# Optimization experiments

Measured on AMD Instinct MI355X. Metric: run time of the kernel, lower is better.

Reference implementation:

```python
import jax, jax.numpy as jnp
import numpy as np

T_CONST = 0.1

def _hardtanh(w):
    # F.hardtanh(w, min_val=1e-10, max_val=1)
    return jnp.clip(w, 1e-10, 1.0)

def _forward(inp, hn, w_str2str, w_str2snr, w_m12m1, w_m12str, w_thal2m1,
             w_m12thal, w_thal2str, w_str2stn, w_stn2snr, w_snr2thal,
             str2str_fixed, inp_weight, mean_w, mean_b, std_w, std_b, hid_dim):
    H = hid_dim
    H5 = 5 * H
    Z = jnp.zeros((H, H), dtype=inp.dtype)
    n_inhib = int(0.3 * H)

    # Diagonal 'D' matrices realized as column scalings (D is diagonal)
    m12m1_d = jnp.concatenate([jnp.ones((H - n_inhib,)), -jnp.ones((n_inhib,))])

    # Block masks
    str2str_mask = jnp.zeros((H, H))
    m12str_mask = jnp.concatenate([jnp.ones((H, H - n_inhib)), jnp.zeros((H, n_inhib))], axis=1)
    str2stn_mask = jnp.concatenate([jnp.zeros((H, H // 2)), jnp.ones((H, H // 2))], axis=1)
    str2snr_mask = jnp.concatenate([jnp.ones((H, H // 2)), jnp.zeros((H, H // 2))], axis=1)

    # Region masks over the full 5H state
    thal_mask = jnp.concatenate([jnp.zeros((3 * H,)), jnp.ones((H,)), jnp.zeros((H,))])
    m1_mask = jnp.zeros((H5,))  # cat(zeros(4H), zeros(H)) in the source

    # Effective recurrent blocks (str2str_D = stn2snr_D = snr2thal_D = str2snr_D = -I)
    str2str_rec = -(str2str_mask * _hardtanh(w_str2str) + str2str_fixed)
    m12m1_rec = _hardtanh(w_m12m1) * m12m1_d[None, :]
    m12str_rec = m12str_mask * _hardtanh(w_m12str)
    str2snr_rec = -(str2snr_mask * _hardtanh(w_str2snr))
    thal2m1_rec = _hardtanh(w_thal2m1)
    m12thal_rec = _hardtanh(w_m12thal)
    thal2str_rec = _hardtanh(w_thal2str)
    str2stn_rec = str2stn_mask * _hardtanh(w_str2stn)
    stn2snr_rec = -_hardtanh(w_str2stn)  # NOTE: source uses str2stn weight here (faithful to original)
    snr2thal_rec = -_hardtanh(w_snr2thal)

    W_rec = jnp.concatenate([
        jnp.concatenate([str2str_rec, Z, Z, thal2str_rec, m12str_rec], axis=1),
        jnp.concatenate([str2stn_rec, Z, Z, Z, Z], axis=1),
        jnp.concatenate([str2snr_rec, stn2snr_rec, Z, Z, Z], axis=1),
        jnp.concatenate([Z, Z, snr2thal_rec, Z, m12thal_rec], axis=1),
        jnp.concatenate([Z, Z, Z, thal2m1_rec, m12m1_rec], axis=1),
    ], axis=0)  # [5H, 5H]

    # Precompute masked input drive for all timesteps: [T, B, 5H]
    u = jnp.einsum('bti,ih->tbh', inp, _hardtanh(inp_weight)) * thal_mask

    W_rec_T = W_rec.T

    def step(h, u_t):
        # (W_rec @ h.T).T == h @ W_rec.T
        h_new = jax.nn.relu((1.0 - T_CONST) * h + T_CONST * (h @ W_rec_T + u_t))
        return h_new, h_new

    _, hs = jax.lax.scan(step, hn[0], u)  # hs: [T, B, 5H]
    rnn_out = jnp.transpose(hs, (1, 0, 2))  # [B, T, 5H]
    hn_last = rnn_out[:, -1, :][None]  # [1, B, 5H]

    masked = rnn_out * m1_mask
    mean_out = masked @ mean_w + mean_b
    std_out = jnp.clip(masked @ std_w + std_b, -5.0, 10.0)
    return mean_out, std_out, rnn_out, hn_last


def setup_inputs() -> dict:
    H, B, T, I, A = 256, 64, 512, 4, 1
    H5 = 5 * H
    key = jax.random.key(0)
    ks = jax.random.split(key, 20)
    u01 = lambda k, shape, s: jax.random.uniform(k, shape, dtype=jnp.float32) * s
    inputs = {
        'inp': jax.random.uniform(ks[0], (B, T, I), dtype=jnp.float32),
        'hn': jnp.zeros((1, B, H5), dtype=jnp.float32),
        'w_str2str': u01(ks[1], (H, H), 0.01),
        'w_str2snr': u01(ks[2], (H, H), 0.01),
        'w_m12m1': u01(ks[3], (H, H), 0.01),
        'w_m12str': u01(ks[4], (H, H), 0.01),
        'w_thal2m1': u01(ks[5], (H, H), 0.01),
        'w_m12thal': u01(ks[6], (H, H), 0.01),
        'w_thal2str': u01(ks[7], (H, H), 0.01),
        'w_str2stn': u01(ks[8], (H, H), 0.01),
        'w_stn2snr': u01(ks[9], (H, H), 0.01),
        'w_snr2thal': u01(ks[10], (H, H), 0.01),
        'inp_weight': u01(ks[12], (I, H5), 0.1),
        'mean_w': jax.random.normal(ks[13], (H5, A), dtype=jnp.float32) * 0.02,
        'mean_b': jnp.zeros((A,), dtype=jnp.float32),
        'std_w': jax.random.normal(ks[14], (H5, A), dtype=jnp.float32) * 0.02,
        'std_b': jnp.zeros((A,), dtype=jnp.float32),
        'hid_dim': H,
    }
    keep = jax.random.bernoulli(ks[11], 0.15, (H, H)).astype(jnp.float32)
    inputs['str2str_fixed'] = u01(ks[15], (H, H), 0.01) * keep
    return inputs


def reference(inp, hn, w_str2str, w_str2snr, w_m12m1, w_m12str, w_thal2m1,
              w_m12thal, w_thal2str, w_str2stn, w_stn2snr, w_snr2thal,
              str2str_fixed, inp_weight, mean_w, mean_b, std_w, std_b, hid_dim):
    return _forward(inp, hn, w_str2str, w_str2snr, w_m12m1, w_m12str, w_thal2m1,
                    w_m12thal, w_thal2str, w_str2stn, w_stn2snr, w_snr2thal,
                    str2str_fixed, inp_weight, mean_w, mean_b, std_w, std_b, hid_dim)
```

## Files before the change

### kernel.cpp

```cpp
#include <hip/hip_runtime.h>

typedef unsigned short u16;
typedef unsigned long long u64;
typedef __bf16 v8bf __attribute__((ext_vector_type(8)));
typedef float f32x4 __attribute__((ext_vector_type(4)));
typedef u16 u16x4 __attribute__((ext_vector_type(4)));

#define H5 1280
#define TT 512
#define NBLK 80
#define GBLK 20
#define SPL 81920

#define OFF_W0 0
#define OFF_W1 3276800
#define OFF_W2 6553600
#define OFF_HS 9830400
#define OFF_WIN 10813440
#define OFF_CNT 10817536

#define MFMA(a, b, c) __builtin_amdgcn_mfma_f32_16x16x32_bf16(a, b, c, 0, 0, 0)

__device__ __forceinline__ float htanh_(float x) {
  return fminf(fmaxf(x, 1e-10f), 1.0f);
}
__device__ __forceinline__ u16 f2b(float f) {
  unsigned u = __float_as_uint(f);
  return (u16)((u + 0x7fffu + ((u >> 16) & 1u)) >> 16);
}
__device__ __forceinline__ float b2f(u16 b) {
  return __uint_as_float(((unsigned)b) << 16);
}

__device__ __forceinline__ v8bf ldh16(const u16* p) {
  v8bf v;
  asm volatile("global_load_dwordx4 %0, %1, off sc0 sc1" : "=v"(v) : "v"(p) : "memory");
  return v;
}
__device__ __forceinline__ void sth(u16* p, u16x4 v) {
  union { u16x4 s; u64 q; } u;
  u.s = v;
  __hip_atomic_store((u64*)p, u.q, __ATOMIC_RELAXED, __HIP_MEMORY_SCOPE_AGENT);
}

__global__ void build_w(const float* __restrict__ w_str2snr, const float* __restrict__ w_m12m1,
                        const float* __restrict__ w_m12str, const float* __restrict__ w_thal2m1,
                        const float* __restrict__ w_m12thal, const float* __restrict__ w_thal2str,
                        const float* __restrict__ w_str2stn, const float* __restrict__ w_snr2thal,
                        const float* __restrict__ fixedw, u16* __restrict__ W0,
                        u16* __restrict__ W1, u16* __restrict__ W2) {
  int idx = blockIdx.x * 256 + threadIdx.x;
  if (idx >= H5 * H5) return;
  int j = idx / H5, k = idx - j * H5;
  int jr = j >> 8, kr = k >> 8, kk = k & 255;
  int o = (j & 255) * 256 + kk;
  float w = 0.0f;
  if (jr == 0) {
    if (kr == 0) w = -fixedw[o];
    else if (kr == 3) w = htanh_(w_thal2str[o]);
    else if (kr == 4) w = (kk < 180) ? htanh_(w_m12str[o]) : 0.0f;
  } else if (jr == 1) {
    if (kr == 0) w = (kk >= 128) ? htanh_(w_str2stn[o]) : 0.0f;
  } else if (jr == 2) {
    if (kr == 0) w = (kk < 128) ? -htanh_(w_str2snr[o]) : 0.0f;
    else if (kr == 1) w = -htanh_(w_str2stn[o]);
  } else if (jr == 3) {
    if (kr == 2) w = -htanh_(w_snr2thal[o]);
    else if (kr == 4) w = htanh_(w_m12thal[o]);
  } else {
    if (kr == 3) w = htanh_(w_thal2m1[o]);
    else if (kr == 4) w = (kk < 180) ? htanh_(w_m12m1[o]) : -htanh_(w_m12m1[o]);
  }
  u16 c0 = f2b(w);  float r1 = w - b2f(c0);
  u16 c1 = f2b(r1); float r2 = r1 - b2f(c1);
  u16 c2 = f2b(r2);
  W0[idx] = c0; W1[idx] = c1; W2[idx] = c2;
}

__global__ void build_misc(const float* __restrict__ hn, const float* __restrict__ inp_weight,
                           const float* __restrict__ mean_b, const float* __restrict__ std_b,
                           float* __restrict__ out, u16* __restrict__ hs, float* __restrict__ Win) {
  int gid = blockIdx.x * 256 + threadIdx.x;
  if (gid < 65536) {
    out[gid] = (gid < 32768) ? mean_b[0] : fminf(10.0f, fmaxf(-5.0f, std_b[0]));
  } else if (gid < 65536 + SPL) {
    int i = gid - 65536;
    float v = hn[i];
    u16 c0 = f2b(v);  float r1 = v - b2f(c0);
    u16 c1 = f2b(r1); float r2 = r1 - b2f(c1);
    u16 c2 = f2b(r2);
    hs[i] = c0; hs[SPL + i] = c1; hs[2 * SPL + i] = c2;
  } else if (gid < 65536 + SPL + 1024) {
    int i = gid - 65536 - SPL;
    Win[i] = htanh_(inp_weight[(i >> 8) * H5 + 768 + (i & 255)]);
  }
}

template <int R> struct RC;
template <> struct RC<0> { static constexpr int kb[3] = {0, 768, 1024}; static constexpr int nch[3] = {8, 8, 8}; };
template <> struct RC<1> { static constexpr int kb[3] = {128, 0, 0};    static constexpr int nch[3] = {4, 0, 0}; };
template <> struct RC<2> { static constexpr int kb[3] = {0, 256, 0};    static constexpr int nch[3] = {4, 8, 0}; };
template <> struct RC<3> { static constexpr int kb[3] = {512, 1024, 0}; static constexpr int nch[3] = {8, 8, 0}; };
template <> struct RC<4> { static constexpr int kb[3] = {768, 1024, 0}; static constexpr int nch[3] = {8, 8, 0}; };

template <int R>
__device__ __forceinline__ f32x4 do_mm(const u16* __restrict__ hs_r, int b, int lk,
                                       const u16* __restrict__ w0r, const u16* __restrict__ w1r,
                                       const u16* __restrict__ w2r) {
  f32x4 A00 = {0.f, 0.f, 0.f, 0.f}, A01 = {0.f, 0.f, 0.f, 0.f}, A02 = {0.f, 0.f, 0.f, 0.f};
  f32x4 A10 = {0.f, 0.f, 0.f, 0.f}, A11 = {0.f, 0.f, 0.f, 0.f}, A20 = {0.f, 0.f, 0.f, 0.f};
#pragma unroll
  for (int q = 0; q < 3; ++q) {
    if (RC<R>::nch[q] > 0) {
      const int kbq = RC<R>::kb[q];
      const u16* hb = hs_r + (long)b * H5 + kbq + lk;
      v8bf h0[8], h1[8], h2[8];
#pragma unroll
      for (int c = 0; c < RC<R>::nch[q]; ++c) {
        h0[c] = ldh16(hb + c * 32);
        h1[c] = ldh16(hb + SPL + c * 32);
        h2[c] = ldh16(hb + 2 * SPL + c * 32);
      }
      asm volatile("s_waitcnt vmcnt(0)" ::: "memory");
      __builtin_amdgcn_sched_barrier(0);
#pragma unroll
      for (int c = 0; c < RC<R>::nch[q]; ++c) {
        v8bf a0 = *(const v8bf*)(w0r + kbq + c * 32);
        v8bf a1 = *(const v8bf*)(w1r + kbq + c * 32);
        v8bf a2 = *(const v8bf*)(w2r + kbq + c * 32);
        A00 = MFMA(a0, h0[c], A00);
        A01 = MFMA(a0, h1[c], A01);
        A02 = MFMA(a0, h2[c], A02);
        A10 = MFMA(a1, h0[c], A10);
        A11 = MFMA(a1, h1[c], A11);
        A20 = MFMA(a2, h0[c], A20);
      }
    }
  }
  f32x4 acc;
#pragma unroll
  for (int rr = 0; rr < 4; ++rr)
    acc[rr] = ((A00[rr] + A10[rr]) + (A01[rr] + A11[rr])) + (A02[rr] + A20[rr]);
  return acc;
}

template <int R>
__device__ void pers_loop(int j0, int b, int lr, int hi, int lk,
                          const float* __restrict__ inp_b, const float* __restrict__ hn,
                          const u16* __restrict__ W0, const u16* __restrict__ W1,
                          const u16* __restrict__ W2, u16* __restrict__ hs,
                          float* __restrict__ rnn_b, float* __restrict__ hn_last,
                          const float* __restrict__ Win, unsigned* __restrict__ ctr) {
  const long jrow = (long)(j0 + lr) * H5 + lk;
  const u16* w0r = W0 + jrow;
  const u16* w1r = W1 + jrow;
  const u16* w2r = W2 + jrow;

  float winreg[4][4];
  if constexpr (R == 3) {
#pragma unroll
    for (int i = 0; i < 4; ++i)
#pragma unroll
      for (int rr = 0; rr < 4; ++rr)
        winreg[i][rr] = Win[i * 256 + (j0 - 768) + hi * 4 + rr];
  }

  f32x4 hprev;
  {
    const float* hp = hn + (long)b * H5 + j0 + hi * 4;
#pragma unroll
    for (int rr = 0; rr < 4; ++rr) hprev[rr] = hp[rr];
  }

  const u64 ca = (u64)ctr;

  for (int t = 0; t < TT; ++t) {
    const u16* hs_r = hs + (t & 1) * (3 * SPL);
    u16* hs_w = hs + ((t & 1) ^ 1) * (3 * SPL);

    f32x4 acc = do_mm<R>(hs_r, b, lk, w0r, w1r, w2r);

    if constexpr (R == 3) {
      const float* ip = inp_b + t * 4;
      float i0 = ip[0], i1 = ip[1], i2 = ip[2], i3 = ip[3];
#pragma unroll
      for (int rr = 0; rr < 4; ++rr)
        acc[rr] += i0 * winreg[0][rr] + i1 * winreg[1][rr] + i2 * winreg[2][rr] + i3 * winreg[3][rr];
    }

    f32x4 hnew;
#pragma unroll
    for (int rr = 0; rr < 4; ++rr)
      hnew[rr] = fmaxf(0.0f, 0.9f * hprev[rr] + 0.1f * acc[rr]);
    hprev = hnew;

    *(f32x4*)(rnn_b + (long)t * H5 + j0 + hi * 4) = hnew;

    if (t < TT - 1) {
      u16x4 s0, s1, s2;
#pragma unroll
      for (int rr = 0; rr < 4; ++rr) {
        float v = hnew[rr];
        u16 c0 = f2b(v);  float r1 = v - b2f(c0);
        u16 c1 = f2b(r1); float r2 = r1 - b2f(c1);
        s0[rr] = c0; s1[rr] = c1; s2[rr] = f2b(r2);
      }
      u16* hw = hs_w + (long)b * H5 + j0 + hi * 4;
      sth(hw, s0);
      sth(hw + SPL, s1);
      sth(hw + 2 * SPL, s2);

      asm volatile("s_waitcnt vmcnt(0)" ::: "memory");
      __syncthreads();
      if (threadIdx.x == 0) {
        unsigned old;
        asm volatile("global_atomic_add %0, %1, %2, off sc0 sc1\n\t"
                     "s_waitcnt vmcnt(0)"
                     : "=v"(old) : "v"(ca), "v"(1u) : "memory");
        const unsigned target = (unsigned)(t + 1) * GBLK;
        for (;;) {
          unsigned cur;
          asm volatile("global_load_dword %0, %1, off sc0 sc1\n\t"
                       "s_waitcnt vmcnt(0)"
                       : "=v"(cur) : "v"(ca) : "memory");
          if (cur >= target) break;
          __builtin_amdgcn_s_sleep(2);
        }
      }
      __syncthreads();
    } else {
      float* hl = hn_last + (long)b * H5 + j0 + hi * 4;
#pragma unroll
      for (int rr = 0; rr < 4; ++rr) hl[rr] = hnew[rr];
    }
  }
}

__global__ void __launch_bounds__(256, 1)
rnn_pers(const float* __restrict__ inp, const float* __restrict__ hn,
         const u16* __restrict__ W0, const u16* __restrict__ W1, const u16* __restrict__ W2,
         u16* __restrict__ hs, float* __restrict__ rnn, float* __restrict__ hn_last,
         const float* __restrict__ Win, unsigned* __restrict__ cnt, int cstride) {
  const int lane = threadIdx.x & 63;
  const int lr = lane & 15, hi = lane >> 4, lk = hi * 8;
  const int g = blockIdx.x & 3;
  const int i = blockIdx.x >> 2;
  const int w = threadIdx.x >> 6;
  const int jt = i * 4 + w;
  const int j0 = jt << 4;
  const int b = (g << 4) + lr;
  unsigned* ctr = cnt + g * cstride;
  float* rnn_b = rnn + (long)b * TT * H5;
  const float* inp_b = inp + (long)b * TT * 4;
  switch (i >> 2) {
    case 0: pers_loop<0>(j0, b, lr, hi, lk, inp_b, hn, W0, W1, W2, hs, rnn_b, hn_last, Win, ctr); break;
    case 1: pers_loop<1>(j0, b, lr, hi, lk, inp_b, hn, W0, W1, W2, hs, rnn_b, hn_last, Win, ctr); break;
    case 2: pers_loop<2>(j0, b, lr, hi, lk, inp_b, hn, W0, W1, W2, hs, rnn_b, hn_last, Win, ctr); break;
    case 3: pers_loop<3>(j0, b, lr, hi, lk, inp_b, hn, W0, W1, W2, hs, rnn_b, hn_last, Win, ctr); break;
    default: pers_loop<4>(j0, b, lr, hi, lk, inp_b, hn, W0, W1, W2, hs, rnn_b, hn_last, Win, ctr); break;
  }
}

template <int R>
__device__ void step_one(int t, int j0, int b, int lr, int hi, int lk,
                         const float* __restrict__ inp_b, const float* __restrict__ hn,
                         const u16* __restrict__ W0, const u16* __restrict__ W1,
                         const u16* __restrict__ W2, u16* __restrict__ hs,
                         float* __restrict__ rnn, float* __restrict__ rnn_b,
                         float* __restrict__ hn_last, const float* __restrict__ Win) {
  const long jrow = (long)(j0 + lr) * H5 + lk;
  const u16* hs_r = hs + (t & 1) * (3 * SPL);
  u16* hs_w = hs + ((t & 1) ^ 1) * (3 * SPL);

  f32x4 acc = do_mm<R>(hs_r, b, lk, W0 + jrow, W1 + jrow, W2 + jrow);

  if constexpr (R == 3) {
    float winreg[4][4];
#pragma unroll
    for (int i = 0; i < 4; ++i)
#pragma unroll
      for (int rr = 0; rr < 4; ++rr)
        winreg[i][rr] = Win[i * 256 + (j0 - 768) + hi * 4 + rr];
    const float* ip = inp_b + t * 4;
    float i0 = ip[0], i1 = ip[1], i2 = ip[2], i3 = ip[3];
#pragma unroll
    for (int rr = 0; rr < 4; ++rr)
      acc[rr] += i0 * winreg[0][rr] + i1 * winreg[1][rr] + i2 * winreg[2][rr] + i3 * winreg[3][rr];
  }

  f32x4 hprev;
  {
    const float* hp = (t == 0) ? (hn + (long)b * H5 + j0 + hi * 4)
                               : (rnn + ((long)b * TT + (t - 1)) * H5 + j0 + hi * 4);
#pragma unroll
    for (int rr = 0; rr < 4; ++rr) hprev[rr] = hp[rr];
  }
  f32x4 hnew;
#pragma unroll
  for (int rr = 0; rr < 4; ++rr)
    hnew[rr] = fmaxf(0.0f, 0.9f * hprev[rr] + 0.1f * acc[rr]);

  *(f32x4*)(rnn_b + (long)t * H5 + j0 + hi * 4) = hnew;
  if (t < TT - 1) {
    u16x4 s0, s1, s2;
#pragma unroll
    for (int rr = 0; rr < 4; ++rr) {
      float v = hnew[rr];
      u16 c0 = f2b(v);  float r1 = v - b2f(c0);
      u16 c1 = f2b(r1); float r2 = r1 - b2f(c1);
      s0[rr] = c0; s1[rr] = c1; s2[rr] = f2b(r2);
    }
    u16* hw = hs_w + (long)b * H5 + j0 + hi * 4;
    sth(hw, s0);
    sth(hw + SPL, s1);
    sth(hw + 2 * SPL, s2);
  } else {
    float* hl = hn_last + (long)b * H5 + j0 + hi * 4;
#pragma unroll
    for (int rr = 0; rr < 4; ++rr) hl[rr] = hnew[rr];
  }
}

__global__ void __launch_bounds__(256, 1)
rnn_step(const float* __restrict__ inp, const float* __restrict__ hn,
         const u16* __restrict__ W0, const u16* __restrict__ W1, const u16* __restrict__ W2,
         u16* __restrict__ hs, float* __restrict__ rnn, float* __restrict__ hn_last,
         const float* __restrict__ Win, int t) {
  const int lane = threadIdx.x & 63;
  const int lr = lane & 15, hi = lane >> 4, lk = hi * 8;
  const int g = blockIdx.x & 3;
  const int i = blockIdx.x >> 2;
  const int w = threadIdx.x >> 6;
  const int jt = i * 4 + w;
  const int j0 = jt << 4;
  const int b = (g << 4) + lr;
  float* rnn_b = rnn + (long)b * TT * H5;
  const float* inp_b = inp + (long)b * TT * 4;
  switch (i >> 2) {
    case 0: step_one<0>(t, j0, b, lr, hi, lk, inp_b, hn, W0, W1, W2, hs, rnn, rnn_b, hn_last, Win); break;
    case 1: step_one<1>(t, j0, b, lr, hi, lk, inp_b, hn, W0, W1, W2, hs, rnn, rnn_b, hn_last, Win); break;
    case 2: step_one<2>(t, j0, b, lr, hi, lk, inp_b, hn, W0, W1, W2, hs, rnn, rnn_b, hn_last, Win); break;
    case 3: step_one<3>(t, j0, b, lr, hi, lk, inp_b, hn, W0, W1, W2, hs, rnn, rnn_b, hn_last, Win); break;
    default: step_one<4>(t, j0, b, lr, hi, lk, inp_b, hn, W0, W1, W2, hs, rnn, rnn_b, hn_last, Win); break;
  }
}

extern "C" void kernel_launch(void* const* d_in, const int* in_sizes, int n_in,
                              void* d_out, int out_size, void* d_ws, size_t ws_size,
                              hipStream_t stream) {
  const float* inp        = (const float*)d_in[0];
  const float* hn         = (const float*)d_in[1];
  const float* w_str2snr  = (const float*)d_in[3];
  const float* w_m12m1    = (const float*)d_in[4];
  const float* w_m12str   = (const float*)d_in[5];
  const float* w_thal2m1  = (const float*)d_in[6];
  const float* w_m12thal  = (const float*)d_in[7];
  const float* w_thal2str = (const float*)d_in[8];
  const float* w_str2stn  = (const float*)d_in[9];
  const float* w_snr2thal = (const float*)d_in[11];
  const float* inp_weight = (const float*)d_in[12];
  const float* mean_b     = (const float*)d_in[14];
  const float* std_b      = (const float*)d_in[16];
  const float* fixedw     = (const float*)d_in[18];

  char* ws = (char*)d_ws;
  u16* W0 = (u16*)(ws + OFF_W0);
  u16* W1 = (u16*)(ws + OFF_W1);
  u16* W2 = (u16*)(ws + OFF_W2);
  u16* hsb = (u16*)(ws + OFF_HS);
  float* Win = (float*)(ws + OFF_WIN);
  unsigned* cnt = (unsigned*)(ws + OFF_CNT);

  int cstride;
  size_t cbytes;
  if (ws_size >= (size_t)OFF_CNT + 1024) { cstride = 64; cbytes = 1024; }
  else                                   { cstride = 8;  cbytes = 128;  }

  float* out = (float*)d_out;
  float* rnn = out + 65536;
  float* hnl = out + 65536 + 41943040;

  hipMemsetAsync(cnt, 0, cbytes, stream);
  build_w<<<6400, 256, 0, stream>>>(w_str2snr, w_m12m1, w_m12str, w_thal2m1, w_m12thal,
                                    w_thal2str, w_str2stn, w_snr2thal, fixedw, W0, W1, W2);
  build_misc<<<581, 256, 0, stream>>>(hn, inp_weight, mean_b, std_b, out, hsb, Win);

  void* args[] = {(void*)&inp, (void*)&hn, (void*)&W0, (void*)&W1, (void*)&W2, (void*)&hsb,
                  (void*)&rnn, (void*)&hnl, (void*)&Win, (void*)&cnt, (void*)&cstride};
  hipError_t e = hipLaunchCooperativeKernel((const void*)rnn_pers, dim3(NBLK), dim3(256),
                                            args, 0, stream);
  if (e != hipSuccess) {
    for (int t = 0; t < TT; ++t)
      rnn_step<<<NBLK, 256, 0, stream>>>(inp, hn, W0, W1, W2, hsb, rnn, hnl, Win, t);
  }
}
```

Before: 8.959 ms.

## Replace atomic counter barrier with per-block flag array and relax cache scopes

The grid barrier in the persistent RNN kernel changes from an atomic-add counter to per-block flag stores. Each waiter reads all 20 flags of its group with vector loads and takes the minimum. Hidden-state loads and stores drop the sc0 bit and use plain sc1-scoped stores instead of agent-scope atomics, and the fallback per-step kernel uses ordinary loads and stores. The intent is to remove atomic serialization and cut barrier latency per timestep. The risk is memory visibility across CUs if sc1 alone is not coherent enough, and the smaller-workspace flag stride changes.

```diff
diff --git a/kernel.cpp b/kernel.cpp
--- a/kernel.cpp
+++ b/kernel.cpp
@@ -2,9 +2,11 @@
 
 typedef unsigned short u16;
 typedef unsigned long long u64;
+typedef unsigned u32;
 typedef __bf16 v8bf __attribute__((ext_vector_type(8)));
 typedef float f32x4 __attribute__((ext_vector_type(4)));
 typedef u16 u16x4 __attribute__((ext_vector_type(4)));
+typedef u32 u32x4 __attribute__((ext_vector_type(4)));
 
 #define H5 1280
 #define TT 512
@@ -34,14 +36,15 @@
 
 __device__ __forceinline__ v8bf ldh16(const u16* p) {
   v8bf v;
-  asm volatile("global_load_dwordx4 %0, %1, off sc0 sc1" : "=v"(v) : "v"(p) : "memory");
+  asm volatile("global_load_dwordx4 %0, %1, off sc1" : "=v"(v) : "v"(p) : "memory");
   return v;
 }
 __device__ __forceinline__ void sth(u16* p, u16x4 v) {
   union { u16x4 s; u64 q; } u;
   u.s = v;
-  __hip_atomic_store((u64*)p, u.q, __ATOMIC_RELAXED, __HIP_MEMORY_SCOPE_AGENT);
-}
+  asm volatile("global_store_dwordx2 %0, %1, off sc1" :: "v"(p), "v"(u.q) : "memory");
+}
+__device__ __forceinline__ u32 umin_(u32 a, u32 b) { return a < b ? a : b; }
 
 __global__ void build_w(const float* __restrict__ w_str2snr, const float* __restrict__ w_m12m1,
                         const float* __restrict__ w_m12str, const float* __restrict__ w_thal2m1,
@@ -103,7 +106,7 @@
 template <> struct RC<3> { static constexpr int kb[3] = {512, 1024, 0}; static constexpr int nch[3] = {8, 8, 0}; };
 template <> struct RC<4> { static constexpr int kb[3] = {768, 1024, 0}; static constexpr int nch[3] = {8, 8, 0}; };
 
-template <int R>
+template <int R, bool SC>
 __device__ __forceinline__ f32x4 do_mm(const u16* __restrict__ hs_r, int b, int lk,
                                        const u16* __restrict__ w0r, const u16* __restrict__ w1r,
                                        const u16* __restrict__ w2r) {
@@ -117,12 +120,20 @@
       v8bf h0[8], h1[8], h2[8];
 #pragma unroll
       for (int c = 0; c < RC<R>::nch[q]; ++c) {
-        h0[c] = ldh16(hb + c * 32);
-        h1[c] = ldh16(hb + SPL + c * 32);
-        h2[c] = ldh16(hb + 2 * SPL + c * 32);
+        if constexpr (SC) {
+          h0[c] = ldh16(hb + c * 32);
+          h1[c] = ldh16(hb + SPL + c * 32);
+          h2[c] = ldh16(hb + 2 * SPL + c * 32);
+        } else {
+          h0[c] = *(const v8bf*)(hb + c * 32);
+          h1[c] = *(const v8bf*)(hb + SPL + c * 32);
+          h2[c] = *(const v8bf*)(hb + 2 * SPL + c * 32);
+        }
       }
-      asm volatile("s_waitcnt vmcnt(0)" ::: "memory");
-      __builtin_amdgcn_sched_barrier(0);
+      if constexpr (SC) {
+        asm volatile("s_waitcnt vmcnt(0)" ::: "memory");
+        __builtin_amdgcn_sched_barrier(0);
+      }
 #pragma unroll
       for (int c = 0; c < RC<R>::nch[q]; ++c) {
         v8bf a0 = *(const v8bf*)(w0r + kbq + c * 32);
@@ -145,12 +156,12 @@
 }
 
 template <int R>
-__device__ void pers_loop(int j0, int b, int lr, int hi, int lk,
+__device__ void pers_loop(int j0, int b, int lr, int hi, int lk, int slot,
                           const float* __restrict__ inp_b, const float* __restrict__ hn,
                           const u16* __restrict__ W0, const u16* __restrict__ W1,
                           const u16* __restrict__ W2, u16* __restrict__ hs,
                           float* __restrict__ rnn_b, float* __restrict__ hn_last,
-                          const float* __restrict__ Win, unsigned* __restrict__ ctr) {
+                          const float* __restrict__ Win, u32* __restrict__ flags) {
   const long jrow = (long)(j0 + lr) * H5 + lk;
   const u16* w0r = W0 + jrow;
   const u16* w1r = W1 + jrow;
@@ -172,13 +183,11 @@
     for (int rr = 0; rr < 4; ++rr) hprev[rr] = hp[rr];
   }
 
-  const u64 ca = (u64)ctr;
-
   for (int t = 0; t < TT; ++t) {
     const u16* hs_r = hs + (t & 1) * (3 * SPL);
     u16* hs_w = hs + ((t & 1) ^ 1) * (3 * SPL);
 
-    f32x4 acc = do_mm<R>(hs_r, b, lk, w0r, w1r, w2r);
+    f32x4 acc = do_mm<R, true>(hs_r, b, lk, w0r, w1r, w2r);
 
     if constexpr (R == 3) {
       const float* ip = inp_b + t * 4;
@@ -213,17 +222,24 @@
       asm volatile("s_waitcnt vmcnt(0)" ::: "memory");
       __syncthreads();
       if (threadIdx.x == 0) {
-        unsigned old;
-        asm volatile("global_atomic_add %0, %1, %2, off sc0 sc1\n\t"
-                     "s_waitcnt vmcnt(0)"
-                     : "=v"(old) : "v"(ca), "v"(1u) : "memory");
-        const unsigned target = (unsigned)(t + 1) * GBLK;
+        u32 tv = (u32)(t + 1);
+        u32* myf = flags + slot;
+        asm volatile("global_store_dword %0, %1, off sc1\n\t"
+                     "s_waitcnt vmcnt(0)" :: "v"(myf), "v"(tv) : "memory");
         for (;;) {
-          unsigned cur;
-          asm volatile("global_load_dword %0, %1, off sc0 sc1\n\t"
-                       "s_waitcnt vmcnt(0)"
-                       : "=v"(cur) : "v"(ca) : "memory");
-          if (cur >= target) break;
+          u32x4 f0, f1, f2, f3, f4;
+          asm volatile("global_load_dwordx4 %0, %1, off sc1" : "=v"(f0) : "v"(flags) : "memory");
+          asm volatile("global_load_dwordx4 %0, %1, off sc1" : "=v"(f1) : "v"(flags + 4) : "memory");
+          asm volatile("global_load_dwordx4 %0, %1, off sc1" : "=v"(f2) : "v"(flags + 8) : "memory");
+          asm volatile("global_load_dwordx4 %0, %1, off sc1" : "=v"(f3) : "v"(flags + 12) : "memory");
+          asm volatile("global_load_dwordx4 %0, %1, off sc1" : "=v"(f4) : "v"(flags + 16) : "memory");
+          asm volatile("s_waitcnt vmcnt(0)" ::: "memory");
+          u32 m = umin_(umin_(umin_(f0[0], f0[1]), umin_(f0[2], f0[3])),
+                        umin_(umin_(f1[0], f1[1]), umin_(f1[2], f1[3])));
+          m = umin_(m, umin_(umin_(f2[0], f2[1]), umin_(f2[2], f2[3])));
+          m = umin_(m, umin_(umin_(f3[0], f3[1]), umin_(f3[2], f3[3])));
+          m = umin_(m, umin_(umin_(f4[0], f4[1]), umin_(f4[2], f4[3])));
+          if (m >= tv) break;
           __builtin_amdgcn_s_sleep(2);
         }
       }
@@ -240,7 +256,7 @@
 rnn_pers(const float* __restrict__ inp, const float* __restrict__ hn,
          const u16* __restrict__ W0, const u16* __restrict__ W1, const u16* __restrict__ W2,
          u16* __restrict__ hs, float* __restrict__ rnn, float* __restrict__ hn_last,
-         const float* __restrict__ Win, unsigned* __restrict__ cnt, int cstride) {
+         const float* __restrict__ Win, u32* __restrict__ cnt, int cstride) {
   const int lane = threadIdx.x & 63;
   const int lr = lane & 15, hi = lane >> 4, lk = hi * 8;
   const int g = blockIdx.x & 3;
@@ -249,15 +265,15 @@
   const int jt = i * 4 + w;
   const int j0 = jt << 4;
   const int b = (g << 4) + lr;
-  unsigned* ctr = cnt + g * cstride;
+  u32* flags = cnt + g * cstride;
   float* rnn_b = rnn + (long)b * TT * H5;
   const float* inp_b = inp + (long)b * TT * 4;
   switch (i >> 2) {
-    case 0: pers_loop<0>(j0, b, lr, hi, lk, inp_b, hn, W0, W1, W2, hs, rnn_b, hn_last, Win, ctr); break;
-    case 1: pers_loop<1>(j0, b, lr, hi, lk, inp_b, hn, W0, W1, W2, hs, rnn_b, hn_last, Win, ctr); break;
-    case 2: pers_loop<2>(j0, b, lr, hi, lk, inp_b, hn, W0, W1, W2, hs, rnn_b, hn_last, Win, ctr); break;
-    case 3: pers_loop<3>(j0, b, lr, hi, lk, inp_b, hn, W0, W1, W2, hs, rnn_b, hn_last, Win, ctr); break;
-    default: pers_loop<4>(j0, b, lr, hi, lk, inp_b, hn, W0, W1, W2, hs, rnn_b, hn_last, Win, ctr); break;
+    case 0: pers_loop<0>(j0, b, lr, hi, lk, i, inp_b, hn, W0, W1, W2, hs, rnn_b, hn_last, Win, flags); break;
+    case 1: pers_loop<1>(j0, b, lr, hi, lk, i, inp_b, hn, W0, W1, W2, hs, rnn_b, hn_last, Win, flags); break;
+    case 2: pers_loop<2>(j0, b, lr, hi, lk, i, inp_b, hn, W0, W1, W2, hs, rnn_b, hn_last, Win, flags); break;
+    case 3: pers_loop<3>(j0, b, lr, hi, lk, i, inp_b, hn, W0, W1, W2, hs, rnn_b, hn_last, Win, flags); break;
+    default: pers_loop<4>(j0, b, lr, hi, lk, i, inp_b, hn, W0, W1, W2, hs, rnn_b, hn_last, Win, flags); break;
   }
 }
 
@@ -272,7 +288,7 @@
   const u16* hs_r = hs + (t & 1) * (3 * SPL);
   u16* hs_w = hs + ((t & 1) ^ 1) * (3 * SPL);
 
-  f32x4 acc = do_mm<R>(hs_r, b, lk, W0 + jrow, W1 + jrow, W2 + jrow);
+  f32x4 acc = do_mm<R, false>(hs_r, b, lk, W0 + jrow, W1 + jrow, W2 + jrow);
 
   if constexpr (R == 3) {
     float winreg[4][4];
@@ -311,9 +327,9 @@
       s0[rr] = c0; s1[rr] = c1; s2[rr] = f2b(r2);
     }
     u16* hw = hs_w + (long)b * H5 + j0 + hi * 4;
-    sth(hw, s0);
-    sth(hw + SPL, s1);
-    sth(hw + 2 * SPL, s2);
+    *(u16x4*)(hw) = s0;
+    *(u16x4*)(hw + SPL) = s1;
+    *(u16x4*)(hw + 2 * SPL) = s2;
   } else {
     float* hl = hn_last + (long)b * H5 + j0 + hi * 4;
 #pragma unroll
@@ -369,12 +385,12 @@
   u16* W2 = (u16*)(ws + OFF_W2);
   u16* hsb = (u16*)(ws + OFF_HS);
   float* Win = (float*)(ws + OFF_WIN);
-  unsigned* cnt = (unsigned*)(ws + OFF_CNT);
+  u32* cnt = (u32*)(ws + OFF_CNT);
 
   int cstride;
   size_t cbytes;
   if (ws_size >= (size_t)OFF_CNT + 1024) { cstride = 64; cbytes = 1024; }
-  else                                   { cstride = 8;  cbytes = 128;  }
+  else                                   { cstride = 32; cbytes = 512;  }
 
   float* out = (float*)d_out;
   float* rnn = out + 65536;
```

New measurement: 9.103 ms. No clear change (+1.6%).
